# Performance work log

Hardware: AMD Instinct MI355X
Metric: run time of the kernel (lower is better)

## Reference

```python
import jax, jax.numpy as jnp
import numpy as np
import math

HIDDEN = 2048
NUM_HEADS = 16
HEAD_SIZE = HIDDEN // NUM_HEADS
BATCH = 2
SEQ = 2048


def setup_inputs() -> dict:
    key = jax.random.key(0)
    k_x, k_wq, k_bq, k_wo, k_bo = jax.random.split(key, 5)
    scale_in = 1.0 / math.sqrt(HIDDEN)
    return {
        "x": jax.random.normal(k_x, (BATCH, SEQ, HIDDEN), dtype=jnp.float32),
        # torch Linear stored as W[out,in]; we keep the jax-friendly transpose [in,out]
        "Wqkv": jax.random.normal(k_wq, (HIDDEN, 3 * HIDDEN), dtype=jnp.float32) * scale_in,
        "bqkv": jax.random.normal(k_bq, (3 * HIDDEN,), dtype=jnp.float32) * 0.01,
        "Wo": jax.random.normal(k_wo, (HIDDEN, HIDDEN), dtype=jnp.float32) * scale_in,
        "bo": jax.random.normal(k_bo, (HIDDEN,), dtype=jnp.float32) * 0.01,
    }


def reference(x, Wqkv, bqkv, Wo, bo):
    b, s, _ = x.shape
    # fused QKV projection; channel layout is (three, num_heads, head_size)
    kqv = x @ Wqkv + bqkv                      # [b, s, 3*hidden]
    kqv = kqv.reshape(b, s, 3, NUM_HEADS, HEAD_SIZE)
    q = kqv[:, :, 0]                           # [b, s, n, h]
    k = kqv[:, :, 1]
    v = kqv[:, :, 2]
    # scores[b, n, s_key, t_query] = K_s . Q_t, scaled
    scores = jnp.einsum('bsnh,btnh->bnst', k, q) / math.sqrt(HEAD_SIZE)
    # faithful to original: keep upper triangle (key <= query), masked entries are exactly -10000
    ones = jnp.ones_like(scores)
    scores = jnp.triu(scores) + (-10000.0) * jnp.tril(ones, k=-1)
    attn = jax.nn.softmax(scores, axis=2)      # softmax over key dim
    out = jnp.einsum('bnkq,bknh->bqnh', attn, v)  # [b, s, n, h]
    out = out.reshape(b, s, NUM_HEADS * HEAD_SIZE)
    return out @ Wo + bo
```

## Files before the change

### kernel.cpp

```cpp
#include <hip/hip_runtime.h>
#include <hip/hip_bf16.h>

typedef __hip_bfloat16 bf16;
typedef __attribute__((ext_vector_type(8))) short short8;
typedef __attribute__((ext_vector_type(8))) unsigned short ushort8;
typedef __attribute__((ext_vector_type(4))) float floatx4;

#define BATCH 2
#define S_LEN 2048
#define NHEAD 16
#define HD 128
#define HIDDEN 2048
#define QSCALE 0.12754435f
#define FOFF 12.0f

static __device__ __forceinline__ unsigned short f2bf(float f) {
    union { float f; unsigned int u; } c; c.f = f;
    unsigned int u = c.u;
    unsigned int rounded = u + 0x7FFF + ((u >> 16) & 1);
    return (unsigned short)(rounded >> 16);
}

static __device__ __forceinline__ short8 lds_read16(unsigned off) {
    short8 r;
    asm volatile("ds_read_b128 %0, %1" : "=v"(r) : "v"(off));
    return r;
}

__global__ __launch_bounds__(256) void cast_f32_bf16(const float* __restrict__ src,
                                                     bf16* __restrict__ dst) {
    int i = (blockIdx.x * 256 + threadIdx.x) * 8;
    float4 a = *(const float4*)&src[i];
    float4 b = *(const float4*)&src[i + 4];
    ushort8 o;
    o[0] = f2bf(a.x); o[1] = f2bf(a.y); o[2] = f2bf(a.z); o[3] = f2bf(a.w);
    o[4] = f2bf(b.x); o[5] = f2bf(b.y); o[6] = f2bf(b.z); o[7] = f2bf(b.w);
    *(ushort8*)&dst[i] = o;
}

__global__ __launch_bounds__(256) void cast_transpose(const float* __restrict__ src,
                                                      bf16* __restrict__ dst,
                                                      int R, int C) {
    __shared__ unsigned short t[32][33];
    int tx = threadIdx.x & 31, ty = threadIdx.x >> 5;
    int c0 = blockIdx.x * 32, r0 = blockIdx.y * 32;
#pragma unroll
    for (int i = 0; i < 4; i++) {
        int r = r0 + ty + i * 8;
        t[ty + i * 8][tx] = f2bf(src[(size_t)r * C + c0 + tx]);
    }
    __syncthreads();
#pragma unroll
    for (int i = 0; i < 4; i++) {
        int cc = c0 + ty + i * 8;
        ((unsigned short*)dst)[(size_t)cc * R + r0 + tx] = t[tx][ty + i * 8];
    }
}

#define GK 2048
#define NT 32

#define STG(pG, lG, s, h)                                                       \
    do {                                                                        \
        __builtin_amdgcn_global_load_lds(                                       \
            (const __attribute__((address_space(1))) void*)(pG + (size_t)((h) * 128) * GK + (s) * 64), \
            (__attribute__((address_space(3))) void*)(lG + ((s) & 1) * 32768 + (h) * 16384 + ldst),    \
            16, 0, 0);                                                          \
        __builtin_amdgcn_global_load_lds(                                       \
            (const __attribute__((address_space(1))) void*)(pG + (size_t)((h) * 128 + 64) * GK + (s) * 64), \
            (__attribute__((address_space(3))) void*)(lG + ((s) & 1) * 32768 + (h) * 16384 + 8192 + ldst), \
            16, 0, 0);                                                          \
    } while (0)

#define LDAo(i, ks) lds_read16(Ab + ((unsigned)(wm * 128 + (i) * 16 + lr) << 7) + ((((ks) * 64 + quad * 16)) ^ axor))
#define LDBo(j, ks) lds_read16(Bb + ((unsigned)(wn * 64 + (j) * 16 + lr) << 7) + ((((ks) * 64 + quad * 16)) ^ axor))

#define PHASE_MFMA(IOFF, BF, JOFF)                                              \
    __builtin_amdgcn_s_setprio(1);                                              \
    _Pragma("unroll")                                                           \
    for (int ks = 0; ks < 2; ks++)                                              \
        _Pragma("unroll")                                                       \
        for (int i = 0; i < 4; i++)                                             \
            _Pragma("unroll")                                                   \
            for (int j = 0; j < 2; j++)                                         \
                acc[(IOFF) + i][(JOFF) + j] = __builtin_amdgcn_mfma_f32_16x16x32_bf16( \
                    aF[i][ks], BF[j][ks], acc[(IOFF) + i][(JOFF) + j], 0, 0, 0); \
    __builtin_amdgcn_s_setprio(0);

#define BAR __builtin_amdgcn_s_barrier()
#define LGKM0 asm volatile("s_waitcnt lgkmcnt(0)" ::: "memory")
#define SCHED0 __builtin_amdgcn_sched_barrier(0)

template <int EPI>
__global__ __launch_bounds__(512, 2) void gemm256(const bf16* __restrict__ A,
                                                  const bf16* __restrict__ Bt,
                                                  const float* __restrict__ bias,
                                                  bf16* __restrict__ Qb,
                                                  bf16* __restrict__ Kb,
                                                  bf16* __restrict__ Vt,
                                                  float* __restrict__ Cout,
                                                  int ntN) {
    __shared__ __align__(16) bf16 Asm[2][256 * 64];
    __shared__ __align__(16) bf16 Bsm[2][256 * 64];

    int tid = threadIdx.x;
    int wave = tid >> 6, lane = tid & 63;
    int quad = lane >> 4, lr = lane & 15;
    int wm = wave >> 2, wn = wave & 3;
    unsigned axor = (unsigned)((lr & 7) << 4);

    int nwg = gridDim.x;
    int cpx = nwg >> 3;
    int bid = blockIdx.x;
    int swz = (bid & 7) * cpx + (bid >> 3);
    int mt = swz / ntN, nt = swz - mt * ntN;
    int m0 = mt * 256, n0 = nt * 256;

    int srow = wave * 8 + (lane >> 3);
    int scol = ((lane & 7) ^ ((lane >> 3) & 7)) * 8;
    const bf16* pA = A + (size_t)(m0 + srow) * GK + scol;
    const bf16* pB = Bt + (size_t)(n0 + srow) * GK + scol;
    char* lA = (char*)&Asm[0][0];
    char* lB = (char*)&Bsm[0][0];
    int ldst = wave * 1024;

    unsigned aBase0 = (unsigned)(size_t)(__attribute__((address_space(3))) char*)lA;
    unsigned bBase0 = (unsigned)(size_t)(__attribute__((address_space(3))) char*)lB;

    const floatx4 fzero = {0.f, 0.f, 0.f, 0.f};
    floatx4 acc[8][4];
#pragma unroll
    for (int i = 0; i < 8; i++)
#pragma unroll
        for (int j = 0; j < 4; j++) acc[i][j] = fzero;

    short8 aF[4][2], b0F[2][2], b1F[2][2];

    STG(pB, lB, 0, 0); STG(pB, lB, 0, 1); STG(pA, lA, 0, 0); STG(pA, lA, 0, 1);
    STG(pB, lB, 1, 0); STG(pB, lB, 1, 1); STG(pA, lA, 1, 0); STG(pA, lA, 1, 1);
    asm volatile("s_waitcnt vmcnt(8)" ::: "memory");
    BAR;

    for (int t = 0; t < NT; ++t) {
        unsigned Ab = aBase0 + (unsigned)((t & 1) * 32768);
        unsigned Bb = bBase0 + (unsigned)((t & 1) * 32768);

#pragma unroll
        for (int i = 0; i < 4; i++) { aF[i][0] = LDAo(i, 0); aF[i][1] = LDAo(i, 1); }
#pragma unroll
        for (int j = 0; j < 2; j++) { b0F[j][0] = LDBo(j, 0); b0F[j][1] = LDBo(j, 1); }
        BAR; LGKM0; SCHED0;
        PHASE_MFMA(0, b0F, 0)
        BAR;

#pragma unroll
        for (int j = 0; j < 2; j++) { b1F[j][0] = LDBo(j + 2, 0); b1F[j][1] = LDBo(j + 2, 1); }
        BAR; LGKM0; SCHED0;
        PHASE_MFMA(0, b1F, 2)
        BAR;

#pragma unroll
        for (int i = 0; i < 4; i++) { aF[i][0] = LDAo(i + 4, 0); aF[i][1] = LDAo(i + 4, 1); }
        if (t + 2 < NT) { STG(pB, lB, t + 2, 0); STG(pB, lB, t + 2, 1); }
        BAR; LGKM0; SCHED0;
        PHASE_MFMA(4, b1F, 2)
        BAR;

        if (t + 2 < NT) {
            STG(pA, lA, t + 2, 0); STG(pA, lA, t + 2, 1);
            asm volatile("s_waitcnt vmcnt(8)" ::: "memory");
        } else {
            asm volatile("s_waitcnt vmcnt(0)" ::: "memory");
        }
        BAR;
        PHASE_MFMA(4, b0F, 0)
        BAR;
    }

    if (EPI == 0) {
#pragma unroll
        for (int i = 0; i < 8; i++) {
#pragma unroll
            for (int j = 0; j < 4; j++) {
                int gcn = n0 + wn * 64 + j * 16 + lr;
                float bv = bias[gcn];
                int tsel = gcn >> 11, hh = (gcn >> 7) & 15, d = gcn & 127;
#pragma unroll
                for (int reg = 0; reg < 4; reg++) {
                    int gm = m0 + wm * 128 + i * 16 + quad * 4 + reg;
                    float v = acc[i][j][reg] + bv;
                    int bb = gm >> 11, s = gm & 2047;
                    size_t hb = (size_t)(bb * NHEAD + hh);
                    if (tsel == 0) {
                        Qb[(hb * S_LEN + s) * HD + d] = __float2bfloat16(v * QSCALE);
                    } else if (tsel == 1) {
                        Kb[(hb * S_LEN + s) * HD + d] = __float2bfloat16(v);
                    } else {
                        Vt[(hb * HD + d) * S_LEN + s] = __float2bfloat16(v);
                    }
                }
            }
        }
    } else {
        int N = ntN << 8;
#pragma unroll
        for (int i = 0; i < 8; i++) {
#pragma unroll
            for (int j = 0; j < 4; j++) {
                int gcn = n0 + wn * 64 + j * 16 + lr;
                float bv = bias[gcn];
#pragma unroll
                for (int reg = 0; reg < 4; reg++) {
                    int gm = m0 + wm * 128 + i * 16 + quad * 4 + reg;
                    Cout[(size_t)gm * N + gcn] = acc[i][j][reg] + bv;
                }
            }
        }
    }
}

#define PSTR 72
__global__ __launch_bounds__(256, 2) void attn_kernel(const bf16* __restrict__ Qb,
                                                      const bf16* __restrict__ Kb,
                                                      const bf16* __restrict__ Vt,
                                                      bf16* __restrict__ Obuf) {
    __shared__ __align__(16) bf16 Ks[64 * 128];
    __shared__ __align__(16) bf16 Vs[128 * 64];
    __shared__ __align__(16) bf16 Ps[4][16 * PSTR];

    int tid = threadIdx.x;
    int wave = tid >> 6, lane = tid & 63;
    int quad = lane >> 4, lr = lane & 15;
    int srow = lane >> 4;
    int head = blockIdx.x, p = blockIdx.y, b = blockIdx.z;
    size_t hb = (size_t)(b * NHEAD + head);
    const bf16* Qbase = Qb + hb * S_LEN * HD;
    const bf16* Kbase = Kb + hb * S_LEN * HD;
    const bf16* Vbase = Vt + hb * (size_t)HD * S_LEN;

    const floatx4 fzero = {0.f, 0.f, 0.f, 0.f};
    const float MASKV = -30000.f;
    short8 ones;
#pragma unroll
    for (int i = 0; i < 8; i++) ones[i] = (short)0x3F80;

    for (int sub = 0; sub < 2; sub++) {
        int qt = sub ? (31 - p) : p;
        int q0 = qt * 64;
        int niter = qt + 1;

        short8 qF[4];
#pragma unroll
        for (int kc = 0; kc < 4; kc++)
            qF[kc] = *(const short8*)&Qbase[(size_t)(q0 + wave * 16 + lr) * HD + kc * 32 + quad * 8];

        floatx4 Oacc[8];
        floatx4 lacc = fzero;
#pragma unroll
        for (int dn = 0; dn < 8; dn++) Oacc[dn] = fzero;

        ushort8 kpre[4], vpre[4];
#pragma unroll
        for (int i = 0; i < 4; i++) {
            int rl = wave * 16 + i * 4 + srow;
            int gc = lr ^ (rl & 15);
            kpre[i] = *(const ushort8*)&Kbase[(size_t)rl * HD + gc * 8];
            int vr = wave * 32 + i * 8 + (lane >> 3);
            int gvc = (lane & 7) ^ (vr & 7);
            vpre[i] = *(const ushort8*)&Vbase[(size_t)vr * S_LEN + gvc * 8];
        }

        for (int kt = 0; kt < niter; kt++) {
            __syncthreads();
#pragma unroll
            for (int i = 0; i < 4; i++) {
                *(ushort8*)&Ks[(wave * 16 + i * 4) * 128 + lane * 8] = kpre[i];
                *(ushort8*)&Vs[(wave * 32 + i * 8) * 64 + lane * 8] = vpre[i];
            }
            __syncthreads();
            if (kt + 1 < niter) {
                int ns0 = (kt + 1) * 64;
#pragma unroll
                for (int i = 0; i < 4; i++) {
                    int rl = wave * 16 + i * 4 + srow;
                    int gc = lr ^ (rl & 15);
                    kpre[i] = *(const ushort8*)&Kbase[(size_t)(ns0 + rl) * HD + gc * 8];
                    int vr = wave * 32 + i * 8 + (lane >> 3);
                    int gvc = (lane & 7) ^ (vr & 7);
                    vpre[i] = *(const ushort8*)&Vbase[(size_t)vr * S_LEN + ns0 + gvc * 8];
                }
            }

            floatx4 sc[4];
#pragma unroll
            for (int nt = 0; nt < 4; nt++) sc[nt] = fzero;
#pragma unroll
            for (int kc = 0; kc < 4; kc++)
#pragma unroll
                for (int nt = 0; nt < 4; nt++) {
                    short8 kf = *(const short8*)&Ks[(nt * 16 + lr) * 128 + (((kc * 4 + quad) ^ lr) & 15) * 8];
                    sc[nt] = __builtin_amdgcn_mfma_f32_16x16x32_bf16(qF[kc], kf, sc[nt], 0, 0, 0);
                }
            if (kt == niter - 1) {
#pragma unroll
                for (int nt = 0; nt < 4; nt++)
#pragma unroll
                    for (int reg = 0; reg < 4; reg++) {
                        int qg = wave * 16 + quad * 4 + reg;
                        int kg = nt * 16 + lr;
                        if (kg > qg) sc[nt][reg] = MASKV;
                    }
            }
#pragma unroll
            for (int nt = 0; nt < 4; nt++)
#pragma unroll
                for (int reg = 0; reg < 4; reg++) {
                    float pv = __builtin_amdgcn_exp2f(sc[nt][reg] - FOFF);
                    Ps[wave][(quad * 4 + reg) * PSTR + nt * 16 + lr] = __float2bfloat16(pv);
                }
#pragma unroll
            for (int st = 0; st < 2; st++) {
                short8 aP = *(const short8*)&Ps[wave][lr * PSTR + st * 32 + quad * 8];
                lacc = __builtin_amdgcn_mfma_f32_16x16x32_bf16(aP, ones, lacc, 0, 0, 0);
#pragma unroll
                for (int dn = 0; dn < 8; dn++) {
                    short8 vf = *(const short8*)&Vs[(dn * 16 + lr) * 64 + (((st * 4 + quad) ^ (lr & 7)) & 7) * 8];
                    Oacc[dn] = __builtin_amdgcn_mfma_f32_16x16x32_bf16(aP, vf, Oacc[dn], 0, 0, 0);
                }
            }
        }

#pragma unroll
        for (int reg = 0; reg < 4; reg++) {
            float inv = 1.0f / lacc[reg];
            int qg = q0 + wave * 16 + quad * 4 + reg;
#pragma unroll
            for (int dn = 0; dn < 8; dn++) {
                int d = dn * 16 + lr;
                Obuf[((size_t)(b * S_LEN + qg)) * HIDDEN + head * HD + d] =
                    __float2bfloat16(Oacc[dn][reg] * inv);
            }
        }
    }
}

extern "C" void kernel_launch(void* const* d_in, const int* in_sizes, int n_in,
                              void* d_out, int out_size, void* d_ws, size_t ws_size,
                              hipStream_t stream) {
    (void)in_sizes; (void)n_in; (void)out_size; (void)ws_size;
    const float* x    = (const float*)d_in[0];
    const float* Wqkv = (const float*)d_in[1];
    const float* bqkv = (const float*)d_in[2];
    const float* Wo   = (const float*)d_in[3];
    const float* bo   = (const float*)d_in[4];
    float* out = (float*)d_out;

    bf16* ws = (bf16*)d_ws;
    bf16* Xb    = ws;
    bf16* Obuf  = ws;
    bf16* WqkvT = ws + (size_t)8388608;
    bf16* WoT   = WqkvT;
    bf16* Qb    = WqkvT + (size_t)12582912;
    bf16* Kb    = Qb + (size_t)8388608;
    bf16* Vt    = Kb + (size_t)8388608;

    cast_f32_bf16<<<4096, 256, 0, stream>>>(x, Xb);
    cast_transpose<<<dim3(192, 64), 256, 0, stream>>>(Wqkv, WqkvT, 2048, 6144);
    gemm256<0><<<dim3(384), dim3(512), 0, stream>>>(Xb, WqkvT, bqkv, Qb, Kb, Vt, nullptr, 24);
    cast_transpose<<<dim3(64, 64), 256, 0, stream>>>(Wo, WoT, 2048, 2048);
    attn_kernel<<<dim3(16, 16, 2), 256, 0, stream>>>(Qb, Kb, Vt, Obuf);
    gemm256<1><<<dim3(128), dim3(512), 0, stream>>>(Obuf, WoT, bo, nullptr, nullptr, nullptr, out, 8);
}
```

Baseline: 414.9 us.

## Replace output projection GEMM with smaller-tile 128x128 kernel for more CTAs

The output projection previously reused the 256x256 pipelined GEMM with only 128 workgroups, which underfills a GPU with 256 CUs. A new simpler 128x128-tile kernel with direct global-to-LDS loads launches 512 workgroups to improve occupancy across CUs. In exchange it loses the double-buffered, software-pipelined schedule and LDS swizzling, so it may suffer bank conflicts and unhidden load latency. The QKV GEMM is de-templated but otherwise unchanged.

```diff
diff --git a/kernel.cpp b/kernel.cpp
--- a/kernel.cpp
+++ b/kernel.cpp
@@ -91,15 +91,13 @@
 #define LGKM0 asm volatile("s_waitcnt lgkmcnt(0)" ::: "memory")
 #define SCHED0 __builtin_amdgcn_sched_barrier(0)
 
-template <int EPI>
-__global__ __launch_bounds__(512, 2) void gemm256(const bf16* __restrict__ A,
-                                                  const bf16* __restrict__ Bt,
-                                                  const float* __restrict__ bias,
-                                                  bf16* __restrict__ Qb,
-                                                  bf16* __restrict__ Kb,
-                                                  bf16* __restrict__ Vt,
-                                                  float* __restrict__ Cout,
-                                                  int ntN) {
+__global__ __launch_bounds__(512, 2) void gemm1_qkv(const bf16* __restrict__ A,
+                                                    const bf16* __restrict__ Bt,
+                                                    const float* __restrict__ bias,
+                                                    bf16* __restrict__ Qb,
+                                                    bf16* __restrict__ Kb,
+                                                    bf16* __restrict__ Vt,
+                                                    int ntN) {
     __shared__ __align__(16) bf16 Asm[2][256 * 64];
     __shared__ __align__(16) bf16 Bsm[2][256 * 64];
 
@@ -177,43 +175,103 @@
         BAR;
     }
 
-    if (EPI == 0) {
-#pragma unroll
-        for (int i = 0; i < 8; i++) {
-#pragma unroll
-            for (int j = 0; j < 4; j++) {
-                int gcn = n0 + wn * 64 + j * 16 + lr;
-                float bv = bias[gcn];
-                int tsel = gcn >> 11, hh = (gcn >> 7) & 15, d = gcn & 127;
-#pragma unroll
-                for (int reg = 0; reg < 4; reg++) {
-                    int gm = m0 + wm * 128 + i * 16 + quad * 4 + reg;
-                    float v = acc[i][j][reg] + bv;
-                    int bb = gm >> 11, s = gm & 2047;
-                    size_t hb = (size_t)(bb * NHEAD + hh);
-                    if (tsel == 0) {
-                        Qb[(hb * S_LEN + s) * HD + d] = __float2bfloat16(v * QSCALE);
-                    } else if (tsel == 1) {
-                        Kb[(hb * S_LEN + s) * HD + d] = __float2bfloat16(v);
-                    } else {
-                        Vt[(hb * HD + d) * S_LEN + s] = __float2bfloat16(v);
-                    }
+#pragma unroll
+    for (int i = 0; i < 8; i++) {
+#pragma unroll
+        for (int j = 0; j < 4; j++) {
+            int gcn = n0 + wn * 64 + j * 16 + lr;
+            float bv = bias[gcn];
+            int tsel = gcn >> 11, hh = (gcn >> 7) & 15, d = gcn & 127;
+#pragma unroll
+            for (int reg = 0; reg < 4; reg++) {
+                int gm = m0 + wm * 128 + i * 16 + quad * 4 + reg;
+                float v = acc[i][j][reg] + bv;
+                int bb = gm >> 11, s = gm & 2047;
+                size_t hb = (size_t)(bb * NHEAD + hh);
+                if (tsel == 0) {
+                    Qb[(hb * S_LEN + s) * HD + d] = __float2bfloat16(v * QSCALE);
+                } else if (tsel == 1) {
+                    Kb[(hb * S_LEN + s) * HD + d] = __float2bfloat16(v);
+                } else {
+                    Vt[(hb * HD + d) * S_LEN + s] = __float2bfloat16(v);
                 }
             }
         }
-    } else {
-        int N = ntN << 8;
-#pragma unroll
-        for (int i = 0; i < 8; i++) {
-#pragma unroll
-            for (int j = 0; j < 4; j++) {
-                int gcn = n0 + wn * 64 + j * 16 + lr;
-                float bv = bias[gcn];
-#pragma unroll
-                for (int reg = 0; reg < 4; reg++) {
-                    int gm = m0 + wm * 128 + i * 16 + quad * 4 + reg;
-                    Cout[(size_t)gm * N + gcn] = acc[i][j][reg] + bv;
-                }
+    }
+}
+
+__global__ __launch_bounds__(256) void gemm_out(const bf16* __restrict__ A,
+                                                const bf16* __restrict__ Bt,
+                                                const float* __restrict__ bias,
+                                                float* __restrict__ C,
+                                                int N, int K) {
+    __shared__ __align__(16) bf16 As[128 * 32];
+    __shared__ __align__(16) bf16 Bs[128 * 32];
+
+    int tid = threadIdx.x;
+    int wave = tid >> 6, lane = tid & 63;
+    int quad = lane >> 4, lr = lane & 15;
+    int wm = wave >> 1, wn = wave & 1;
+    int m0 = blockIdx.y * 128, n0 = blockIdx.x * 128;
+
+    const floatx4 fzero = {0.f, 0.f, 0.f, 0.f};
+    floatx4 acc[4][4];
+#pragma unroll
+    for (int i = 0; i < 4; i++)
+#pragma unroll
+        for (int j = 0; j < 4; j++) acc[i][j] = fzero;
+
+    int rsub = lane >> 2;
+    int csub = (lane & 3) * 8;
+    const bf16* gA0 = A + (size_t)(m0 + wave * 32 + rsub) * K + csub;
+    const bf16* gA1 = gA0 + (size_t)16 * K;
+    const bf16* gB0 = Bt + (size_t)(n0 + wave * 32 + rsub) * K + csub;
+    const bf16* gB1 = gB0 + (size_t)16 * K;
+    bf16* lA0 = As + wave * 1024;
+    bf16* lA1 = As + wave * 1024 + 512;
+    bf16* lB0 = Bs + wave * 1024;
+    bf16* lB1 = Bs + wave * 1024 + 512;
+
+    for (int kt = 0; kt < K; kt += 32) {
+        __builtin_amdgcn_global_load_lds(
+            (const __attribute__((address_space(1))) void*)(gA0 + kt),
+            (__attribute__((address_space(3))) void*)lA0, 16, 0, 0);
+        __builtin_amdgcn_global_load_lds(
+            (const __attribute__((address_space(1))) void*)(gA1 + kt),
+            (__attribute__((address_space(3))) void*)lA1, 16, 0, 0);
+        __builtin_amdgcn_global_load_lds(
+            (const __attribute__((address_space(1))) void*)(gB0 + kt),
+            (__attribute__((address_space(3))) void*)lB0, 16, 0, 0);
+        __builtin_amdgcn_global_load_lds(
+            (const __attribute__((address_space(1))) void*)(gB1 + kt),
+            (__attribute__((address_space(3))) void*)lB1, 16, 0, 0);
+        __syncthreads();
+
+        short8 aF[4], bF[4];
+#pragma unroll
+        for (int i = 0; i < 4; i++)
+            aF[i] = *(const short8*)(As + (wm * 64 + i * 16 + lr) * 32 + quad * 8);
+#pragma unroll
+        for (int j = 0; j < 4; j++)
+            bF[j] = *(const short8*)(Bs + (wn * 64 + j * 16 + lr) * 32 + quad * 8);
+#pragma unroll
+        for (int i = 0; i < 4; i++)
+#pragma unroll
+            for (int j = 0; j < 4; j++)
+                acc[i][j] = __builtin_amdgcn_mfma_f32_16x16x32_bf16(aF[i], bF[j], acc[i][j], 0, 0, 0);
+        __syncthreads();
+    }
+
+#pragma unroll
+    for (int i = 0; i < 4; i++) {
+#pragma unroll
+        for (int j = 0; j < 4; j++) {
+            int gcn = n0 + wn * 64 + j * 16 + lr;
+            float bv = bias[gcn];
+#pragma unroll
+            for (int reg = 0; reg < 4; reg++) {
+                int gm = m0 + wm * 64 + i * 16 + quad * 4 + reg;
+                C[(size_t)gm * N + gcn] = acc[i][j][reg] + bv;
             }
         }
     }
@@ -366,8 +424,8 @@
 
     cast_f32_bf16<<<4096, 256, 0, stream>>>(x, Xb);
     cast_transpose<<<dim3(192, 64), 256, 0, stream>>>(Wqkv, WqkvT, 2048, 6144);
-    gemm256<0><<<dim3(384), dim3(512), 0, stream>>>(Xb, WqkvT, bqkv, Qb, Kb, Vt, nullptr, 24);
+    gemm1_qkv<<<dim3(384), dim3(512), 0, stream>>>(Xb, WqkvT, bqkv, Qb, Kb, Vt, 24);
     cast_transpose<<<dim3(64, 64), 256, 0, stream>>>(Wo, WoT, 2048, 2048);
     attn_kernel<<<dim3(16, 16, 2), 256, 0, stream>>>(Qb, Kb, Vt, Obuf);
-    gemm256<1><<<dim3(128), dim3(512), 0, stream>>>(Obuf, WoT, bo, nullptr, nullptr, nullptr, out, 8);
-}
+    gemm_out<<<dim3(16, 32), 256, 0, stream>>>(Obuf, WoT, bo, out, 2048, 2048);
+}
```

Measured after the change: 405.7 us. -2.2%, faster.
